# Optimization experiments

Hardware: AMD Instinct MI355X
Metric: run time of the kernel (lower is better)

The kernel has to match this reference:

```python
import jax, jax.numpy as jnp
import numpy as np

N = 2048  # device_num
K = 32    # neighbors per device


def setup_inputs() -> dict:
    key = jax.random.key(0)
    k1, k2, k3 = jax.random.split(key, 3)
    dynamic_re = jax.random.uniform(k1, (N, N), dtype=jnp.float32)
    static_re = jax.random.uniform(k2, (N,), dtype=jnp.float32)
    # neighbor ids in [0, N) excluding self (draw in [0, N-1) then shift past row index)
    r = jax.random.randint(k3, (N, K), 0, N - 1)
    rows = jnp.arange(N)[:, None]
    neighbor_matrix = (r + (r >= rows)).astype(jnp.int32)
    return {"dynamic_re": dynamic_re, "static_re": static_re, "neighbor_matrix": neighbor_matrix}


def _trust_forward(dynamic_re, static_re, neighbor_matrix):
    # Semantics of RobustTrustComputing.__call__ on a fresh instance (temp_storage empty):
    #  - diagonal: 1.0
    #  - neighbor (j in nbr(i)): history has len 1 -> CI branch is False -> combined
    #    tau = 0.7*dyn[i,j] + 0.3*stat[j]; prev==combined -> hysteresis takes the
    #    'x <= prev' path: sigmoid(combined + 0.5) with sigmoid(z)=(1-e^-z)/(1+e^-z)=tanh(z/2)
    #  - non-neighbor with common neighbors c: 0.8 * mean_c rep[i,c]*rep[c,j] read from the
    #    PARTIALLY-FILLED matrix in row-major write order (rep[i,c] nonzero only if c<j,
    #    rep[c,j] nonzero only if c<i); divisor is the FULL common-neighbor count.
    #  - non-neighbor, no common neighbors: 0.5*stat[j]
    #  - final clamp to [0,1]
    n = dynamic_re.shape[0]
    idx = jnp.arange(n)
    # membership matrix: M[i, c] True iff c appears in neighbor list of i
    M = jnp.zeros((n, n), dtype=bool).at[idx[:, None], neighbor_matrix].set(True)
    nbrval = jnp.tanh(0.5 * (0.7 * dynamic_re + 0.3 * static_re[None, :] + 0.5))
    Mf = M.astype(dynamic_re.dtype)
    count = Mf @ Mf.T                                  # |common neighbors(i, j)|
    Bmask = Mf.T * (idx[:, None] < idx[None, :])       # [c, j]: c in nbr(j) AND c < j
    fallback = 0.5 * static_re                         # [j]

    def step(rep, xs):
        i, M_i, nbr_i, cnt_i = xs
        # rep[i, c] (c in nbr(i)) equals nbrval[i, c] once column c has been written (c < j,
        # handled by Bmask); rep[c, j] is the final row c only for c < i (rows >= i are zero).
        A = jnp.where(M_i & (idx < i), nbr_i, 0.0)     # [c]
        num = jnp.einsum('c,cj,cj->j', A, rep, Bmask)  # [j]
        indirect = 0.8 * num / jnp.maximum(cnt_i, 1.0)
        row = jnp.where(M_i, nbr_i, jnp.where(cnt_i > 0, indirect, fallback))
        row = jnp.where(idx == i, 1.0, row)            # diagonal overrides everything
        return rep.at[i].set(row), None

    rep0 = jnp.zeros((n, n), dynamic_re.dtype)
    rep, _ = jax.lax.scan(step, rep0, (idx, M, nbrval, count))
    return jnp.clip(rep, 0.0, 1.0)


def reference(dynamic_re, static_re, neighbor_matrix):
    return _trust_forward(dynamic_re, static_re, neighbor_matrix)
```

## Files before the change

### kernel.cpp

```cpp
#include <hip/hip_runtime.h>
#include <math.h>
#include <limits.h>

#define WAVE 64
#define KMAX 32
#define IMAX 96

__device__ __forceinline__ float nvval(float d, float s) {
    return tanhf(0.5f * (0.7f * d + 0.3f * s + 0.5f));
}
__device__ __forceinline__ float clamp01(float x) {
    return fminf(fmaxf(x, 0.0f), 1.0f);
}

__global__ void build_lists(const int* __restrict__ nbr, int N, int K, int W,
                            int* __restrict__ nbrs_sorted, int* __restrict__ deg,
                            unsigned* __restrict__ Mbits, unsigned* __restrict__ Tbits,
                            int* __restrict__ invcnt, int* __restrict__ invlist) {
    int tid = blockIdx.x * blockDim.x + threadIdx.x;
    int i = tid / WAVE;
    int lane = tid % WAVE;
    if (i >= N) return;
    bool have = (lane < K);
    int val = have ? nbr[(size_t)i * K + lane] : INT_MAX;
    bool dup = false;
    for (int t = 0; t < K; ++t) {
        int vt = __shfl(val, t);
        if (have && t < lane && vt == val) dup = true;
    }
    int dupi = (dup || !have) ? 1 : 0;
    int pos = 0;
    for (int t = 0; t < K; ++t) {
        int vt = __shfl(val, t);
        int dt = __shfl(dupi, t);
        if (!dt && vt < val) pos++;
    }
    int myp = (have && !dup) ? pos : -1;
    unsigned long long m = __ballot(have && !dup);
    int degv = __popcll(m);
    int slot = INT_MAX;
    for (int t = 0; t < K; ++t) {
        int pt = __shfl(myp, t);
        int vt = __shfl(val, t);
        if (pt == lane) slot = vt;
    }
    if (lane < K) nbrs_sorted[(size_t)i * K + lane] = slot;
    if (lane == 0) deg[i] = degv;
    if (have) {
        atomicOr(&Mbits[(size_t)i * W + (val >> 5)], 1u << (val & 31));
        atomicOr(&Tbits[(size_t)val * W + (i >> 5)], 1u << (i & 31));
        if (!dup) {
            int p = atomicAdd(&invcnt[val], 1);
            if (p < IMAX) invlist[(size_t)val * IMAX + p] = i;
        }
    }
}

__global__ void __launch_bounds__(256) phase1(
        const float* __restrict__ dyn, const float* __restrict__ stat,
        const int* __restrict__ nbrs_sorted, const int* __restrict__ deg,
        const unsigned* __restrict__ Mbits, const unsigned* __restrict__ Tbits,
        int N, int K, int W, float* __restrict__ out) {
    __shared__ float s_nv[4 * KMAX * KMAX];
    int tid = blockIdx.x * blockDim.x + threadIdx.x;
    int j = tid / WAVE;
    int lane = threadIdx.x & (WAVE - 1);
    int waveid = threadIdx.x >> 6;
    if (j >= N) return;
    int degj = deg[j];
    int c = (lane < K) ? nbrs_sorted[(size_t)j * K + lane] : INT_MAX;
    bool validk = (lane < degj);
    float sk = validk ? stat[c] : 0.0f;
    float statj = stat[j];
    float* s_row = &s_nv[waveid * KMAX * KMAX];

    unsigned dirbit = 0;
    if (validk) {
        unsigned w = Tbits[(size_t)j * W + (c >> 5)];
        dirbit = (w >> (c & 31)) & 1u;
    }
    unsigned dirmask = (unsigned)__ballot(dirbit != 0);
    float dv = 0.0f;
    if (dirbit) dv = nvval(dyn[(size_t)c * N + j], statj);

    unsigned hmAll = 0;
    #pragma unroll
    for (int m = 0; m < KMAX; ++m) {
        int cm = __shfl(c, m);
        if (cm < N) {
            unsigned w = validk ? Mbits[(size_t)cm * W + (c >> 5)] : 0u;
            unsigned b = (w >> (c & 31)) & 1u;
            hmAll |= b << m;
            if (b && lane < m && c < j)
                s_row[m * KMAX + lane] = nvval(dyn[(size_t)cm * N + c], sk);
        }
    }
    unsigned lm = (lane < 31) ? (0xFFFFFFFEu << lane) : 0u;
    unsigned hmTerm = (validk && c < j) ? (hmAll & lm) : 0u;

    int mycnt = 0;
    unsigned H = 0;
    #pragma unroll
    for (int m = 0; m < KMAX; ++m) {
        unsigned long long ball = __ballot((hmAll >> m) & 1u);
        unsigned long long ballT = __ballot((hmTerm >> m) & 1u);
        if (lane == m) mycnt = __popcll(ball);
        H |= (ballT ? 1u : 0u) << m;
    }
    H = __builtin_amdgcn_readfirstlane(H);
    dirmask = __builtin_amdgcn_readfirstlane(dirmask);

    float v = 0.0f;
    #pragma unroll
    for (int m = 0; m < KMAX; ++m) {
        float num = 0.0f;
        if (H & (1u << m)) {
            float t = 0.0f;
            if ((hmTerm >> m) & 1u) t = s_row[m * KMAX + lane] * v;
            num = t;
            num += __shfl_xor(num, 16);
            num += __shfl_xor(num, 8);
            num += __shfl_xor(num, 4);
            num += __shfl_xor(num, 2);
            num += __shfl_xor(num, 1);
        }
        float val;
        if ((dirmask >> m) & 1u) val = dv;
        else if (mycnt > 0) val = 0.8f * num / (float)mycnt;
        else val = 0.5f * statj;
        val = clamp01(val);
        if (lane == m) v = val;
    }
    if (validk) out[(size_t)c * N + j] = v;
}

__global__ void __launch_bounds__(256) phase2(
        const float* __restrict__ dyn, const float* __restrict__ stat,
        const int* __restrict__ nbrs_sorted,
        const unsigned* __restrict__ Mbits, const unsigned* __restrict__ Tbits,
        const int* __restrict__ invcnt, const int* __restrict__ invlist,
        int N, int K, int W, float* __restrict__ out) {
    extern __shared__ char smem[];
    int* s_cnt = (int*)smem;
    float* s_num = (float*)(s_cnt + N);
    unsigned* s_Mw = (unsigned*)(s_num + N);
    unsigned* s_Sw = s_Mw + W;
    int* s_nbr = (int*)(s_Sw + W);
    float* s_nv = (float*)(s_nbr + K);
    int* s_icnt = (int*)(s_nv + K);

    int i = blockIdx.x;
    int tid = threadIdx.x;

    for (int t = tid; t < N; t += blockDim.x) { s_cnt[t] = 0; s_num[t] = 0.0f; }
    if (tid < W) {
        s_Mw[tid] = Mbits[(size_t)i * W + tid];
        s_Sw[tid] = Tbits[(size_t)i * W + tid];
    }
    if (tid < K) {
        int c = nbrs_sorted[(size_t)i * K + tid];
        s_nbr[tid] = c;
        if (c < N) {
            s_nv[tid] = nvval(dyn[(size_t)i * N + c], stat[c]);
            int m = invcnt[c];
            s_icnt[tid] = (m < IMAX) ? m : IMAX;
        } else {
            s_nv[tid] = 0.0f;
            s_icnt[tid] = 0;
        }
    }
    __syncthreads();

    {
        int k = tid >> 3;
        int e0 = tid & 7;
        if (k < K) {
            int c = s_nbr[k];
            int m = s_icnt[k];
            float nv = s_nv[k];
            for (int e = e0; e < m; e += 8) {
                int j = invlist[(size_t)c * IMAX + e];
                atomicAdd(&s_cnt[j], 1);
                if (c < i && c < j)
                    atomicAdd(&s_num[j], nv * out[(size_t)c * N + j]);
            }
        }
    }
    __syncthreads();

    for (int j = tid; j < N; j += blockDim.x) {
        bool skip = ((s_Sw[j >> 5] >> (j & 31)) & 1u) != 0u;
        bool dir  = ((s_Mw[j >> 5] >> (j & 31)) & 1u) != 0u;
        float val;
        if (j == i) {
            val = 1.0f;
        } else if (dir) {
            val = nvval(dyn[(size_t)i * N + j], stat[j]);
        } else {
            int cnt = s_cnt[j];
            val = (cnt > 0) ? (0.8f * s_num[j] / (float)cnt) : (0.5f * stat[j]);
        }
        val = clamp01(val);
        if (!skip) out[(size_t)i * N + j] = val;
    }
}

extern "C" void kernel_launch(void* const* d_in, const int* in_sizes, int n_in,
                              void* d_out, int out_size, void* d_ws, size_t ws_size,
                              hipStream_t stream) {
    const float* dyn = (const float*)d_in[0];
    const float* stat = (const float*)d_in[1];
    const int* nbr = (const int*)d_in[2];
    int N = in_sizes[1];
    int K = in_sizes[2] / N;
    int W = (N + 31) / 32;
    float* out = (float*)d_out;

    char* ws = (char*)d_ws;
    size_t offNbr = 0;
    size_t offDeg = offNbr + (size_t)N * K * sizeof(int);
    size_t offM = offDeg + (size_t)N * sizeof(int);
    size_t offT = offM + (size_t)N * W * sizeof(unsigned);
    size_t offIC = offT + (size_t)N * W * sizeof(unsigned);
    size_t offIL = offIC + (size_t)N * sizeof(int);
    int* nbrs_sorted = (int*)(ws + offNbr);
    int* deg = (int*)(ws + offDeg);
    unsigned* Mbits = (unsigned*)(ws + offM);
    unsigned* Tbits = (unsigned*)(ws + offT);
    int* invcnt = (int*)(ws + offIC);
    int* invlist = (int*)(ws + offIL);

    hipMemsetAsync(ws + offM, 0, offIL - offM, stream);

    int threads = 256;
    int blocksWave = (N * WAVE + threads - 1) / threads;
    build_lists<<<blocksWave, threads, 0, stream>>>(nbr, N, K, W, nbrs_sorted, deg,
                                                    Mbits, Tbits, invcnt, invlist);
    phase1<<<blocksWave, threads, 0, stream>>>(dyn, stat, nbrs_sorted, deg,
                                               Mbits, Tbits, N, K, W, out);
    size_t smem = (size_t)N * 8 + (size_t)W * 8 + (size_t)K * 12;
    phase2<<<N, threads, smem, stream>>>(dyn, stat, nbrs_sorted, Mbits, Tbits,
                                         invcnt, invlist, N, K, W, out);
}
```

Baseline: 127.6 us.

## Store phase1 column values compactly and write output rows densely in phase2

Result: faster. 125.0 us (-2.1%).

```diff
diff --git a/kernel.cpp b/kernel.cpp
--- a/kernel.cpp
+++ b/kernel.cpp
@@ -16,7 +16,8 @@
 __global__ void build_lists(const int* __restrict__ nbr, int N, int K, int W,
                             int* __restrict__ nbrs_sorted, int* __restrict__ deg,
                             unsigned* __restrict__ Mbits, unsigned* __restrict__ Tbits,
-                            int* __restrict__ invcnt, int* __restrict__ invlist) {
+                            int* __restrict__ invcnt, int* __restrict__ invlist,
+                            int* __restrict__ invpos) {
     int tid = blockIdx.x * blockDim.x + threadIdx.x;
     int i = tid / WAVE;
     int lane = tid % WAVE;
@@ -52,6 +53,7 @@
         if (!dup) {
             int p = atomicAdd(&invcnt[val], 1);
             if (p < IMAX) invlist[(size_t)val * IMAX + p] = i;
+            invpos[(size_t)i * K + myp] = p;
         }
     }
 }
@@ -60,7 +62,8 @@
         const float* __restrict__ dyn, const float* __restrict__ stat,
         const int* __restrict__ nbrs_sorted, const int* __restrict__ deg,
         const unsigned* __restrict__ Mbits, const unsigned* __restrict__ Tbits,
-        int N, int K, int W, float* __restrict__ out) {
+        const int* __restrict__ invpos, int N, int K, int W,
+        float* __restrict__ Vcomp) {
     __shared__ float s_nv[4 * KMAX * KMAX];
     int tid = blockIdx.x * blockDim.x + threadIdx.x;
     int j = tid / WAVE;
@@ -131,32 +134,30 @@
         val = clamp01(val);
         if (lane == m) v = val;
     }
-    if (validk) out[(size_t)c * N + j] = v;
+    if (validk) {
+        int p = invpos[(size_t)j * K + lane];
+        if (p < IMAX) Vcomp[(size_t)c * IMAX + p] = v;
+    }
 }
 
 __global__ void __launch_bounds__(256) phase2(
         const float* __restrict__ dyn, const float* __restrict__ stat,
         const int* __restrict__ nbrs_sorted,
-        const unsigned* __restrict__ Mbits, const unsigned* __restrict__ Tbits,
         const int* __restrict__ invcnt, const int* __restrict__ invlist,
-        int N, int K, int W, float* __restrict__ out) {
+        const float* __restrict__ Vcomp,
+        int N, int K, float* __restrict__ out) {
     extern __shared__ char smem[];
     int* s_cnt = (int*)smem;
     float* s_num = (float*)(s_cnt + N);
-    unsigned* s_Mw = (unsigned*)(s_num + N);
-    unsigned* s_Sw = s_Mw + W;
-    int* s_nbr = (int*)(s_Sw + W);
+    int* s_nbr = (int*)(s_num + N);
     float* s_nv = (float*)(s_nbr + K);
     int* s_icnt = (int*)(s_nv + K);
+    __shared__ int s_me;
 
     int i = blockIdx.x;
     int tid = threadIdx.x;
 
     for (int t = tid; t < N; t += blockDim.x) { s_cnt[t] = 0; s_num[t] = 0.0f; }
-    if (tid < W) {
-        s_Mw[tid] = Mbits[(size_t)i * W + tid];
-        s_Sw[tid] = Tbits[(size_t)i * W + tid];
-    }
     if (tid < K) {
         int c = nbrs_sorted[(size_t)i * K + tid];
         s_nbr[tid] = c;
@@ -169,6 +170,10 @@
             s_icnt[tid] = 0;
         }
     }
+    if (tid == 0) {
+        int m = invcnt[i];
+        s_me = (m < IMAX) ? m : IMAX;
+    }
     __syncthreads();
 
     {
@@ -178,30 +183,39 @@
             int c = s_nbr[k];
             int m = s_icnt[k];
             float nv = s_nv[k];
-            for (int e = e0; e < m; e += 8) {
-                int j = invlist[(size_t)c * IMAX + e];
-                atomicAdd(&s_cnt[j], 1);
-                if (c < i && c < j)
-                    atomicAdd(&s_num[j], nv * out[(size_t)c * N + j]);
+            if (c < N) {
+                for (int e = e0; e < m; e += 8) {
+                    int j = invlist[(size_t)c * IMAX + e];
+                    atomicAdd(&s_cnt[j], 1);
+                    if (c < i && c < j)
+                        atomicAdd(&s_num[j], nv * Vcomp[(size_t)c * IMAX + e]);
+                }
             }
         }
     }
     __syncthreads();
 
+    if (tid < K) {
+        int c = s_nbr[tid];
+        if (c < N) { s_cnt[c] = -1; s_num[c] = s_nv[tid]; }
+    }
+    __syncthreads();
+
+    for (int e = tid; e < s_me; e += blockDim.x) {
+        int j = invlist[(size_t)i * IMAX + e];
+        s_cnt[j] = -1;
+        s_num[j] = Vcomp[(size_t)i * IMAX + e];
+    }
+    __syncthreads();
+
     for (int j = tid; j < N; j += blockDim.x) {
-        bool skip = ((s_Sw[j >> 5] >> (j & 31)) & 1u) != 0u;
-        bool dir  = ((s_Mw[j >> 5] >> (j & 31)) & 1u) != 0u;
+        int cnt = s_cnt[j];
         float val;
-        if (j == i) {
-            val = 1.0f;
-        } else if (dir) {
-            val = nvval(dyn[(size_t)i * N + j], stat[j]);
-        } else {
-            int cnt = s_cnt[j];
-            val = (cnt > 0) ? (0.8f * s_num[j] / (float)cnt) : (0.5f * stat[j]);
-        }
-        val = clamp01(val);
-        if (!skip) out[(size_t)i * N + j] = val;
+        if (j == i) val = 1.0f;
+        else if (cnt < 0) val = s_num[j];
+        else if (cnt > 0) val = 0.8f * s_num[j] / (float)cnt;
+        else val = 0.5f * stat[j];
+        out[(size_t)i * N + j] = clamp01(val);
     }
 }
 
@@ -222,23 +236,28 @@
     size_t offM = offDeg + (size_t)N * sizeof(int);
     size_t offT = offM + (size_t)N * W * sizeof(unsigned);
     size_t offIC = offT + (size_t)N * W * sizeof(unsigned);
-    size_t offIL = offIC + (size_t)N * sizeof(int);
+    size_t offIP = offIC + (size_t)N * sizeof(int);
+    size_t offIL = offIP + (size_t)N * K * sizeof(int);
+    size_t offVC = offIL + (size_t)N * IMAX * sizeof(int);
     int* nbrs_sorted = (int*)(ws + offNbr);
     int* deg = (int*)(ws + offDeg);
     unsigned* Mbits = (unsigned*)(ws + offM);
     unsigned* Tbits = (unsigned*)(ws + offT);
     int* invcnt = (int*)(ws + offIC);
+    int* invpos = (int*)(ws + offIP);
     int* invlist = (int*)(ws + offIL);
-
-    hipMemsetAsync(ws + offM, 0, offIL - offM, stream);
+    float* Vcomp = (float*)(ws + offVC);
+
+    hipMemsetAsync(ws + offM, 0, offIP - offM, stream);
 
     int threads = 256;
     int blocksWave = (N * WAVE + threads - 1) / threads;
     build_lists<<<blocksWave, threads, 0, stream>>>(nbr, N, K, W, nbrs_sorted, deg,
-                                                    Mbits, Tbits, invcnt, invlist);
+                                                    Mbits, Tbits, invcnt, invlist,
+                                                    invpos);
     phase1<<<blocksWave, threads, 0, stream>>>(dyn, stat, nbrs_sorted, deg,
-                                               Mbits, Tbits, N, K, W, out);
-    size_t smem = (size_t)N * 8 + (size_t)W * 8 + (size_t)K * 12;
-    phase2<<<N, threads, smem, stream>>>(dyn, stat, nbrs_sorted, Mbits, Tbits,
-                                         invcnt, invlist, N, K, W, out);
-}
+                                               Mbits, Tbits, invpos, N, K, W, Vcomp);
+    size_t smem = (size_t)N * 8 + (size_t)K * 12 + 16;
+    phase2<<<N, threads, smem, stream>>>(dyn, stat, nbrs_sorted,
+                                         invcnt, invlist, Vcomp, N, K, out);
+}
```
